# Performance work log

Measured on AMD Instinct MI355X. Metric: run time of the kernel, lower is better.

## Reference

```python
import jax, jax.numpy as jnp
import numpy as np

B, T, D_IN, H, NC = 256, 512, 40, 128, 7


def _lstm_dir(x, W_ih, W_hh, b):
    # x: [B,T,D]; W_ih: [4H,D]; W_hh: [4H,H]; b: [4H] (b_ih+b_hh combined)
    pre = jnp.einsum('btd,gd->btg', x, W_ih) + b  # [B,T,4H]
    h0 = jnp.zeros((x.shape[0], W_hh.shape[1]), x.dtype)
    c0 = jnp.zeros_like(h0)

    def step(carry, p_t):
        h, c = carry
        g = p_t + h @ W_hh.T  # [B,4H]
        i, f, gg, o = jnp.split(g, 4, axis=-1)  # PyTorch gate order: i,f,g,o
        i = jax.nn.sigmoid(i)
        f = jax.nn.sigmoid(f)
        gg = jnp.tanh(gg)
        o = jax.nn.sigmoid(o)
        c = f * c + i * gg
        h = o * jnp.tanh(c)
        return (h, c), h

    _, hs = jax.lax.scan(step, (h0, c0), jnp.swapaxes(pre, 0, 1))  # [T,B,H]
    return jnp.swapaxes(hs, 0, 1)  # [B,T,H]


def _bilstm_layer(x, Wf, Uf, bf, Wr, Ur, br):
    fwd = _lstm_dir(x, Wf, Uf, bf)
    rev = _lstm_dir(x[:, ::-1], Wr, Ur, br)[:, ::-1]
    return jnp.concatenate([fwd, rev], axis=-1)  # [B,T,2H]


def setup_inputs() -> dict:
    key = jax.random.key(0)
    ks = jax.random.split(key, 20)
    s = 1.0 / np.sqrt(H)  # PyTorch LSTM init scale

    def u(k, shape):
        return jax.random.uniform(k, shape, jnp.float32, -s, s)

    inp = {
        'x': jax.random.normal(ks[0], (B, T, D_IN), jnp.float32),
        # layer 0 (input dim 40)
        'W_ih_l0_f': u(ks[1], (4 * H, D_IN)), 'W_hh_l0_f': u(ks[2], (4 * H, H)), 'b_l0_f': u(ks[3], (4 * H,)),
        'W_ih_l0_r': u(ks[4], (4 * H, D_IN)), 'W_hh_l0_r': u(ks[5], (4 * H, H)), 'b_l0_r': u(ks[6], (4 * H,)),
        # layer 1 (input dim 2H)
        'W_ih_l1_f': u(ks[7], (4 * H, 2 * H)), 'W_hh_l1_f': u(ks[8], (4 * H, H)), 'b_l1_f': u(ks[9], (4 * H,)),
        'W_ih_l1_r': u(ks[10], (4 * H, 2 * H)), 'W_hh_l1_r': u(ks[11], (4 * H, H)), 'b_l1_r': u(ks[12], (4 * H,)),
        # classifier head
        'fc_w': u(ks[13], (NC, 2 * H)), 'fc_b': u(ks[14], (NC,)),
    }
    return inp


def reference(x, W_ih_l0_f, W_hh_l0_f, b_l0_f, W_ih_l0_r, W_hh_l0_r, b_l0_r,
              W_ih_l1_f, W_hh_l1_f, b_l1_f, W_ih_l1_r, W_hh_l1_r, b_l1_r,
              fc_w, fc_b):
    h1 = _bilstm_layer(x, W_ih_l0_f, W_hh_l0_f, b_l0_f, W_ih_l0_r, W_hh_l0_r, b_l0_r)
    h2 = _bilstm_layer(h1, W_ih_l1_f, W_hh_l1_f, b_l1_f, W_ih_l1_r, W_hh_l1_r, b_l1_r)
    last = h2[:, -1, :]  # [B,2H]; dropout is identity at eval time
    return last @ fc_w.T + fc_b  # [B,NC]
```

## Files before the change

kernel.cpp:

```cpp
#include <hip/hip_runtime.h>
#include <hip/hip_bf16.h>

typedef short short8 __attribute__((ext_vector_type(8)));
typedef short short4v __attribute__((ext_vector_type(4)));
typedef float f32x4 __attribute__((ext_vector_type(4)));
typedef __bf16 bf16x8 __attribute__((ext_vector_type(8)));

#define DEVI static __device__ __forceinline__

#if __has_builtin(__builtin_amdgcn_exp2f)
#define EXP2(x) __builtin_amdgcn_exp2f(x)
#else
#define EXP2(x) exp2f(x)
#endif
#if __has_builtin(__builtin_amdgcn_rcpf)
#define RCP(x) __builtin_amdgcn_rcpf(x)
#else
#define RCP(x) (1.0f / (x))
#endif

static constexpr int BB = 256, TT = 512, DIN0 = 40, HH = 128, NCLS = 7;
static constexpr int NB = 16;
static constexpr int NTHR = 512;
static constexpr float L2E = 1.44269504088896f;

DEVI short f2b(float x) {
  union { __hip_bfloat16 h; short s; } u;
  u.h = __float2bfloat16(x);
  return u.s;
}

DEVI bf16x8 as_bf(short8 s) { return __builtin_bit_cast(bf16x8, s); }

template <bool L0>
__global__ __launch_bounds__(NTHR, 2) void lstm_kernel(
    const float* __restrict__ x0, const short* __restrict__ h1_in,
    const float* __restrict__ Wih_f, const float* __restrict__ Whh_f,
    const float* __restrict__ bias_f, const float* __restrict__ Wih_r,
    const float* __restrict__ Whh_r, const float* __restrict__ bias_r,
    short* __restrict__ h1_out, float* __restrict__ h2last) {
  constexpr int K0 = L0 ? 64 : 256;
  constexpr int DI = L0 ? DIN0 : 256;
  constexpr int KT = K0 + HH;
  constexpr int KF = KT / 32;
  constexpr int RS = KT + 8;

  __shared__ short Bbuf[2][NB][RS];

  const int tid = threadIdx.x;
  const int w = tid >> 6;
  const int lane = tid & 63;
  const int lg = lane >> 4;
  const int bcol = lane & 15;
  const int dir = blockIdx.x & 1;
  const int b0 = (blockIdx.x >> 1) * NB;

  const float* __restrict__ Wih = dir ? Wih_r : Wih_f;
  const float* __restrict__ Whh = dir ? Whh_r : Whh_f;
  const float* __restrict__ bias = dir ? bias_r : bias_f;

  short8 wfrag[4][KF];
#pragma unroll
  for (int q = 0; q < 4; ++q) {
    const float scale = (q == 2) ? (2.0f * L2E) : (-L2E);
    const int m = q * HH + w * 16 + bcol;
#pragma unroll
    for (int kk = 0; kk < KF; ++kk) {
      short8 f;
#pragma unroll
      for (int e = 0; e < 8; ++e) {
        const int k = kk * 32 + lg * 8 + e;
        float v = 0.0f;
        if (k < K0) {
          if (k < DI) v = Wih[(size_t)m * DI + k];
        } else {
          v = Whh[(size_t)m * HH + (k - K0)];
        }
        f[e] = f2b(v * scale);
      }
      wfrag[q][kk] = f;
    }
  }

  f32x4 bq[4];
#pragma unroll
  for (int q = 0; q < 4; ++q) {
    const float scale = (q == 2) ? (2.0f * L2E) : (-L2E);
#pragma unroll
    for (int r = 0; r < 4; ++r)
      bq[q][r] = bias[q * HH + w * 16 + lg * 4 + r] * scale;
  }

  for (int i = tid; i < 2 * NB * RS; i += NTHR) (&Bbuf[0][0][0])[i] = 0;
  __syncthreads();

  {
    const int t0 = dir ? (TT - 1) : 0;
    if constexpr (L0) {
      if (tid < 160) {
        const int bl = tid / 10, c4 = tid % 10;
        f32x4 v = *(const f32x4*)(x0 + ((size_t)(b0 + bl) * TT + t0) * DI + c4 * 4);
        short4v o;
        o[0] = f2b(v[0]); o[1] = f2b(v[1]); o[2] = f2b(v[2]); o[3] = f2b(v[3]);
        *(short4v*)&Bbuf[0][bl][c4 * 4] = o;
      }
    } else {
      const int bl = tid >> 5, seg = tid & 31;
      short8 v = *(const short8*)(h1_in + ((size_t)(b0 + bl) * TT + t0) * 256 + seg * 8);
      *(short8*)&Bbuf[0][bl][seg * 8] = v;
    }
  }
  __syncthreads();

  f32x4 cst = {0.f, 0.f, 0.f, 0.f};

  for (int s = 0; s < TT; ++s) {
    const int cur = s & 1;
    const int t = dir ? (TT - 1 - s) : s;
    const bool st = (s + 1 < TT);

    f32x4 xf;
    short8 xh;
    if (st) {
      const int tn = dir ? (TT - 2 - s) : (s + 1);
      if constexpr (L0) {
        if (tid < 160)
          xf = *(const f32x4*)(x0 + ((size_t)(b0 + tid / 10) * TT + tn) * DI + (tid % 10) * 4);
      } else {
        xh = *(const short8*)(h1_in + ((size_t)(b0 + (tid >> 5)) * TT + tn) * 256 + (tid & 31) * 8);
      }
    }

    f32x4 acc[4] = {bq[0], bq[1], bq[2], bq[3]};
#pragma unroll
    for (int kk = 0; kk < KF; ++kk) {
      const bf16x8 bf = as_bf(*(const short8*)&Bbuf[cur][bcol][kk * 32 + lg * 8]);
#pragma unroll
      for (int q = 0; q < 4; ++q)
        acc[q] = __builtin_amdgcn_mfma_f32_16x16x32_bf16(as_bf(wfrag[q][kk]), bf, acc[q], 0, 0, 0);
    }

    if (st) {
      if constexpr (L0) {
        if (tid < 160) {
          short4v o;
          o[0] = f2b(xf[0]); o[1] = f2b(xf[1]); o[2] = f2b(xf[2]); o[3] = f2b(xf[3]);
          *(short4v*)&Bbuf[cur ^ 1][tid / 10][(tid % 10) * 4] = o;
        }
      } else {
        *(short8*)&Bbuf[cur ^ 1][tid >> 5][(tid & 31) * 8] = xh;
      }
    }

    short4v hp;
    f32x4 hf;
#pragma unroll
    for (int r = 0; r < 4; ++r) {
      const float ig = RCP(1.0f + EXP2(acc[0][r]));
      const float fg = RCP(1.0f + EXP2(acc[1][r]));
      float tg = EXP2(acc[2][r]);
      tg = 1.0f - 2.0f * RCP(tg + 1.0f);
      const float og = RCP(1.0f + EXP2(acc[3][r]));
      const float cn = fg * cst[r] + ig * tg;
      cst[r] = cn;
      float tc = EXP2(cn * (2.0f * L2E));
      tc = 1.0f - 2.0f * RCP(tc + 1.0f);
      const float hv = og * tc;
      hf[r] = hv;
      hp[r] = f2b(hv);
    }
    const int j0 = w * 16 + lg * 4;
    *(short4v*)&Bbuf[cur ^ 1][bcol][K0 + j0] = hp;

    if constexpr (L0) {
      *(short4v*)(h1_out + (((size_t)(b0 + bcol) * TT + t) * 256) + dir * HH + j0) = hp;
    } else {
      if ((dir == 0 && s == TT - 1) || (dir == 1 && s == 0)) {
        *(f32x4*)(h2last + (size_t)(b0 + bcol) * 256 + dir * HH + j0) = hf;
      }
    }
    __syncthreads();
  }
}

__global__ void fc_kernel(const float* __restrict__ h2last,
                          const float* __restrict__ fcw,
                          const float* __restrict__ fcb,
                          float* __restrict__ out) {
  const int gid = blockIdx.x * blockDim.x + threadIdx.x;
  if (gid >= BB * NCLS) return;
  const int b = gid / NCLS, n = gid % NCLS;
  const float* hp = h2last + (size_t)b * 256;
  const float* wp = fcw + (size_t)n * 256;
  float s = fcb[n];
#pragma unroll 8
  for (int j = 0; j < 256; ++j) s = fmaf(hp[j], wp[j], s);
  out[gid] = s;
}

extern "C" void kernel_launch(void* const* d_in, const int* in_sizes, int n_in,
                              void* d_out, int out_size, void* d_ws, size_t ws_size,
                              hipStream_t stream) {
  const float* x     = (const float*)d_in[0];
  const float* Wih0f = (const float*)d_in[1];
  const float* Whh0f = (const float*)d_in[2];
  const float* b0f   = (const float*)d_in[3];
  const float* Wih0r = (const float*)d_in[4];
  const float* Whh0r = (const float*)d_in[5];
  const float* b0r   = (const float*)d_in[6];
  const float* Wih1f = (const float*)d_in[7];
  const float* Whh1f = (const float*)d_in[8];
  const float* b1f   = (const float*)d_in[9];
  const float* Wih1r = (const float*)d_in[10];
  const float* Whh1r = (const float*)d_in[11];
  const float* b1r   = (const float*)d_in[12];
  const float* fcw   = (const float*)d_in[13];
  const float* fcb   = (const float*)d_in[14];

  short* h1 = (short*)d_ws;
  float* h2last = (float*)((char*)d_ws + (size_t)BB * TT * 256 * 2);

  lstm_kernel<true><<<dim3(32), dim3(NTHR), 0, stream>>>(
      x, nullptr, Wih0f, Whh0f, b0f, Wih0r, Whh0r, b0r, h1, nullptr);
  lstm_kernel<false><<<dim3(32), dim3(NTHR), 0, stream>>>(
      nullptr, h1, Wih1f, Whh1f, b1f, Wih1r, Whh1r, b1r, nullptr, h2last);
  fc_kernel<<<dim3((BB * NCLS + 255) / 256), dim3(256), 0, stream>>>(
      h2last, fcw, fcb, (float*)d_out);
}
```

Measured before the change: 1.083 ms.

## Split input and recurrent matmuls, precompute next step's input projection off critical path

Separates the LSTM gate matmul into an input-projection part and a recurrent part. The input projection for step s+1 is computed right after step s's h update, so each step's critical path after the barrier only runs the h-dependent MFMAs. The x staging buffer becomes a separate LDS buffer with a 2-deep prefetch and an XOR swizzle for layer 1. The barrier is replaced by an explicit lgkmcnt wait plus s_barrier. This costs extra LDS and registers, and the split only pays off if it actually shortens the serial recurrent chain.

```diff
diff --git a/kernel.cpp b/kernel.cpp
--- a/kernel.cpp
+++ b/kernel.cpp
@@ -32,20 +32,29 @@
 
 DEVI bf16x8 as_bf(short8 s) { return __builtin_bit_cast(bf16x8, s); }
 
-template <bool L0>
-__global__ __launch_bounds__(NTHR, 2) void lstm_kernel(
+DEVI void bar_lgkm() {
+  asm volatile("s_waitcnt lgkmcnt(0)" ::: "memory");
+  __builtin_amdgcn_s_barrier();
+  __builtin_amdgcn_sched_barrier(0);
+}
+
+template <bool IS_L0>
+__global__ __launch_bounds__(NTHR, 2) void lstm2(
     const float* __restrict__ x0, const short* __restrict__ h1_in,
     const float* __restrict__ Wih_f, const float* __restrict__ Whh_f,
     const float* __restrict__ bias_f, const float* __restrict__ Wih_r,
     const float* __restrict__ Whh_r, const float* __restrict__ bias_r,
     short* __restrict__ h1_out, float* __restrict__ h2last) {
-  constexpr int K0 = L0 ? 64 : 256;
-  constexpr int DI = L0 ? DIN0 : 256;
-  constexpr int KT = K0 + HH;
-  constexpr int KF = KT / 32;
-  constexpr int RS = KT + 8;
-
-  __shared__ short Bbuf[2][NB][RS];
+  constexpr int K0 = IS_L0 ? 64 : 256;
+  constexpr int DI = IS_L0 ? DIN0 : 256;
+  constexpr int KFX = K0 / 32;
+  constexpr int KFH = HH / 32;
+  constexpr int RSH = 136;
+  constexpr int XROWB_L0 = 144;
+  constexpr int XBUF = IS_L0 ? (16 * XROWB_L0) : 8192;
+
+  __shared__ short Hb[2][NB][RSH];
+  __shared__ char Xraw[2 * XBUF];
 
   const int tid = threadIdx.x;
   const int w = tid >> 6;
@@ -59,26 +68,32 @@
   const float* __restrict__ Whh = dir ? Whh_r : Whh_f;
   const float* __restrict__ bias = dir ? bias_r : bias_f;
 
-  short8 wfrag[4][KF];
+  auto tmap = [&](int s) { return dir ? (TT - 1 - s) : s; };
+
+  short8 wx[4][KFX];
+  short8 wh[4][KFH];
 #pragma unroll
   for (int q = 0; q < 4; ++q) {
     const float scale = (q == 2) ? (2.0f * L2E) : (-L2E);
     const int m = q * HH + w * 16 + bcol;
 #pragma unroll
-    for (int kk = 0; kk < KF; ++kk) {
+    for (int kk = 0; kk < KFX; ++kk) {
       short8 f;
 #pragma unroll
       for (int e = 0; e < 8; ++e) {
         const int k = kk * 32 + lg * 8 + e;
-        float v = 0.0f;
-        if (k < K0) {
-          if (k < DI) v = Wih[(size_t)m * DI + k];
-        } else {
-          v = Whh[(size_t)m * HH + (k - K0)];
-        }
+        float v = (k < DI) ? Wih[(size_t)m * DI + k] : 0.0f;
         f[e] = f2b(v * scale);
       }
-      wfrag[q][kk] = f;
+      wx[q][kk] = f;
+    }
+#pragma unroll
+    for (int kk = 0; kk < KFH; ++kk) {
+      short8 f;
+#pragma unroll
+      for (int e = 0; e < 8; ++e)
+        f[e] = f2b(Whh[(size_t)m * HH + kk * 32 + lg * 8 + e] * scale);
+      wh[q][kk] = f;
     }
   }
 
@@ -91,65 +106,90 @@
       bq[q][r] = bias[q * HH + w * 16 + lg * 4 + r] * scale;
   }
 
-  for (int i = tid; i < 2 * NB * RS; i += NTHR) (&Bbuf[0][0][0])[i] = 0;
+  for (int i = tid; i < (int)(2 * NB * RSH * 2) / 4; i += NTHR)
+    ((int*)&Hb[0][0][0])[i] = 0;
+  for (int i = tid; i < (int)(2 * XBUF) / 4; i += NTHR) ((int*)Xraw)[i] = 0;
   __syncthreads();
 
-  {
-    const int t0 = dir ? (TT - 1) : 0;
-    if constexpr (L0) {
-      if (tid < 160) {
-        const int bl = tid / 10, c4 = tid % 10;
-        f32x4 v = *(const f32x4*)(x0 + ((size_t)(b0 + bl) * TT + t0) * DI + c4 * 4);
-        short4v o;
-        o[0] = f2b(v[0]); o[1] = f2b(v[1]); o[2] = f2b(v[2]); o[3] = f2b(v[3]);
-        *(short4v*)&Bbuf[0][bl][c4 * 4] = o;
-      }
+  auto ldx = [&](int p, int kk) -> short8 {
+    if constexpr (IS_L0) {
+      return *(const short8*)(Xraw + p * XBUF + bcol * XROWB_L0 + kk * 64 + lg * 16);
     } else {
-      const int bl = tid >> 5, seg = tid & 31;
-      short8 v = *(const short8*)(h1_in + ((size_t)(b0 + bl) * TT + t0) * 256 + seg * 8);
-      *(short8*)&Bbuf[0][bl][seg * 8] = v;
-    }
+      int byte = ((bcol << 9) + (kk << 6) + (lg << 4)) ^ ((bcol & 7) << 4);
+      return *(const short8*)(Xraw + p * XBUF + byte);
+    }
+  };
+
+  const int xr0 = tid / 10, c40 = tid % 10;
+  const int o_swz = (tid << 4) ^ (((tid >> 5) & 7) << 4);
+  const int xr1 = tid >> 5;
+  const int xcb = o_swz & 511;
+  f32x4 xstage_f = {0.f, 0.f, 0.f, 0.f};
+  short8 xstage_h = {0, 0, 0, 0, 0, 0, 0, 0};
+
+  if constexpr (IS_L0) {
+    if (tid < 160) {
+#pragma unroll
+      for (int p = 0; p < 2; ++p) {
+        f32x4 v = *(const f32x4*)(x0 + ((size_t)(b0 + xr0) * TT + tmap(p)) * DI + c40 * 4);
+        short4v o4;
+        o4[0] = f2b(v[0]); o4[1] = f2b(v[1]); o4[2] = f2b(v[2]); o4[3] = f2b(v[3]);
+        *(short4v*)(Xraw + p * XBUF + xr0 * XROWB_L0 + c40 * 8) = o4;
+      }
+      xstage_f = *(const f32x4*)(x0 + ((size_t)(b0 + xr0) * TT + tmap(2)) * DI + c40 * 4);
+    }
+  } else {
+#pragma unroll
+    for (int p = 0; p < 2; ++p) {
+      short8 v = *(const short8*)((const char*)h1_in +
+                  ((((size_t)(b0 + xr1)) * TT + tmap(p)) << 9) + xcb);
+      *(short8*)(Xraw + p * XBUF + tid * 16) = v;
+    }
+    xstage_h = *(const short8*)((const char*)h1_in +
+                ((((size_t)(b0 + xr1)) * TT + tmap(2)) << 9) + xcb);
   }
   __syncthreads();
 
+  f32x4 acc[4] = {bq[0], bq[1], bq[2], bq[3]};
+#pragma unroll
+  for (int kk = 0; kk < KFX; ++kk) {
+    const bf16x8 bx = as_bf(ldx(0, kk));
+#pragma unroll
+    for (int q = 0; q < 4; ++q)
+      acc[q] = __builtin_amdgcn_mfma_f32_16x16x32_bf16(as_bf(wx[q][kk]), bx, acc[q], 0, 0, 0);
+  }
+  __syncthreads();
+
   f32x4 cst = {0.f, 0.f, 0.f, 0.f};
+  const int j0 = w * 16 + lg * 4;
 
   for (int s = 0; s < TT; ++s) {
     const int cur = s & 1;
-    const int t = dir ? (TT - 1 - s) : s;
-    const bool st = (s + 1 < TT);
-
-    f32x4 xf;
-    short8 xh;
-    if (st) {
-      const int tn = dir ? (TT - 2 - s) : (s + 1);
-      if constexpr (L0) {
-        if (tid < 160)
-          xf = *(const f32x4*)(x0 + ((size_t)(b0 + tid / 10) * TT + tn) * DI + (tid % 10) * 4);
-      } else {
-        xh = *(const short8*)(h1_in + ((size_t)(b0 + (tid >> 5)) * TT + tn) * 256 + (tid & 31) * 8);
-      }
-    }
-
-    f32x4 acc[4] = {bq[0], bq[1], bq[2], bq[3]};
-#pragma unroll
-    for (int kk = 0; kk < KF; ++kk) {
-      const bf16x8 bf = as_bf(*(const short8*)&Bbuf[cur][bcol][kk * 32 + lg * 8]);
+
+    if constexpr (IS_L0) {
+      if (tid < 160) {
+        if (s + 2 < TT) {
+          short4v o4;
+          o4[0] = f2b(xstage_f[0]); o4[1] = f2b(xstage_f[1]);
+          o4[2] = f2b(xstage_f[2]); o4[3] = f2b(xstage_f[3]);
+          *(short4v*)(Xraw + cur * XBUF + xr0 * XROWB_L0 + c40 * 8) = o4;
+        }
+        if (s + 3 < TT)
+          xstage_f = *(const f32x4*)(x0 + ((size_t)(b0 + xr0) * TT + tmap(s + 3)) * DI + c40 * 4);
+      }
+    } else {
+      if (s + 2 < TT) *(short8*)(Xraw + cur * XBUF + tid * 16) = xstage_h;
+      if (s + 3 < TT)
+        xstage_h = *(const short8*)((const char*)h1_in +
+                    ((((size_t)(b0 + xr1)) * TT + tmap(s + 3)) << 9) + xcb);
+    }
+
+#pragma unroll
+    for (int kk = 0; kk < KFH; ++kk) {
+      const bf16x8 bh = as_bf(*(const short8*)&Hb[cur][bcol][kk * 32 + lg * 8]);
 #pragma unroll
       for (int q = 0; q < 4; ++q)
-        acc[q] = __builtin_amdgcn_mfma_f32_16x16x32_bf16(as_bf(wfrag[q][kk]), bf, acc[q], 0, 0, 0);
-    }
-
-    if (st) {
-      if constexpr (L0) {
-        if (tid < 160) {
-          short4v o;
-          o[0] = f2b(xf[0]); o[1] = f2b(xf[1]); o[2] = f2b(xf[2]); o[3] = f2b(xf[3]);
-          *(short4v*)&Bbuf[cur ^ 1][tid / 10][(tid % 10) * 4] = o;
-        }
-      } else {
-        *(short8*)&Bbuf[cur ^ 1][tid >> 5][(tid & 31) * 8] = xh;
-      }
+        acc[q] = __builtin_amdgcn_mfma_f32_16x16x32_bf16(as_bf(wh[q][kk]), bh, acc[q], 0, 0, 0);
     }
 
     short4v hp;
@@ -169,17 +209,29 @@
       hf[r] = hv;
       hp[r] = f2b(hv);
     }
-    const int j0 = w * 16 + lg * 4;
-    *(short4v*)&Bbuf[cur ^ 1][bcol][K0 + j0] = hp;
-
-    if constexpr (L0) {
-      *(short4v*)(h1_out + (((size_t)(b0 + bcol) * TT + t) * 256) + dir * HH + j0) = hp;
+    *(short4v*)&Hb[cur ^ 1][bcol][j0] = hp;
+
+    if constexpr (IS_L0) {
+      *(short4v*)(h1_out + (((size_t)(b0 + bcol) * TT + tmap(s)) * 256) + dir * HH + j0) = hp;
     } else {
-      if ((dir == 0 && s == TT - 1) || (dir == 1 && s == 0)) {
+      if ((dir == 0 && s == TT - 1) || (dir == 1 && s == 0))
         *(f32x4*)(h2last + (size_t)(b0 + bcol) * 256 + dir * HH + j0) = hf;
-      }
-    }
-    __syncthreads();
+    }
+
+    if (s + 1 < TT) {
+      f32x4 a0 = bq[0], a1 = bq[1], a2 = bq[2], a3 = bq[3];
+#pragma unroll
+      for (int kk = 0; kk < KFX; ++kk) {
+        const bf16x8 bx = as_bf(ldx(cur ^ 1, kk));
+        a0 = __builtin_amdgcn_mfma_f32_16x16x32_bf16(as_bf(wx[0][kk]), bx, a0, 0, 0, 0);
+        a1 = __builtin_amdgcn_mfma_f32_16x16x32_bf16(as_bf(wx[1][kk]), bx, a1, 0, 0, 0);
+        a2 = __builtin_amdgcn_mfma_f32_16x16x32_bf16(as_bf(wx[2][kk]), bx, a2, 0, 0, 0);
+        a3 = __builtin_amdgcn_mfma_f32_16x16x32_bf16(as_bf(wx[3][kk]), bx, a3, 0, 0, 0);
+      }
+      acc[0] = a0; acc[1] = a1; acc[2] = a2; acc[3] = a3;
+    }
+
+    bar_lgkm();
   }
 }
 
@@ -220,9 +272,9 @@
   short* h1 = (short*)d_ws;
   float* h2last = (float*)((char*)d_ws + (size_t)BB * TT * 256 * 2);
 
-  lstm_kernel<true><<<dim3(32), dim3(NTHR), 0, stream>>>(
+  lstm2<true><<<dim3(32), dim3(NTHR), 0, stream>>>(
       x, nullptr, Wih0f, Whh0f, b0f, Wih0r, Whh0r, b0r, h1, nullptr);
-  lstm_kernel<false><<<dim3(32), dim3(NTHR), 0, stream>>>(
+  lstm2<false><<<dim3(32), dim3(NTHR), 0, stream>>>(
       nullptr, h1, Wih1f, Whh1f, b1f, Wih1r, Whh1r, b1r, nullptr, h2last);
   fc_kernel<<<dim3((BB * NCLS + 255) / 256), dim3(256), 0, stream>>>(
       h2last, fcw, fcb, (float*)d_out);
```

Result: slower. 1.156 ms (+6.8%).
